# Kernel optimization log

Measured on AMD Instinct MI355X. Metric: run time of the kernel, lower is better.

## Reference

```python
import jax, jax.numpy as jnp
import numpy as np

B, N, D, O, K, E = 16, 10000, 128, 64, 3, 160000


def setup_inputs() -> dict:
    key = jax.random.key(0)
    k1, k2, k3, k4, k5 = jax.random.split(key, 5)
    x = jax.random.normal(k1, (B, N, D), dtype=jnp.float32)
    W = jax.random.normal(k2, (K, D, O), dtype=jnp.float32) * (1.0 / np.sqrt(D))
    sup_vals = jax.random.uniform(k3, (K, E), dtype=jnp.float32)
    sup_row = jax.random.randint(k4, (K, E), 0, N, dtype=jnp.int32)
    sup_col = jax.random.randint(k5, (K, E), 0, N, dtype=jnp.int32)
    return {"x": x, "W": W, "sup_vals": sup_vals, "sup_row": sup_row, "sup_col": sup_col}


def reference(x, W, sup_vals, sup_row, sup_col):
    # x: [B, N, D]; W: [K, D, O]; supports as COO edge lists per support.
    # dropout=0.0 (keep_prob=1) -> identity; act=None -> identity; agg='concat'.
    num_nodes = x.shape[1]
    num_supports = W.shape[0]
    outs = []
    for i in range(num_supports):
        # dense feature transform, laid out node-major for the SpMM: [N, B, O]
        pre = jnp.einsum('bnd,do->nbo', x, W[i])
        # SpMM: out[r] += A[r,c] * pre[c]  via gather + segment_sum
        gathered = pre[sup_col[i]] * sup_vals[i][:, None, None]  # [E, B, O]
        agg = jax.ops.segment_sum(gathered, sup_row[i], num_segments=num_nodes)  # [N, B, O]
        outs.append(jnp.transpose(agg, (1, 0, 2)))  # [B, N, O]
    return jnp.concatenate(outs, axis=-1)  # [B, N, O*K]
```

## Files before the change

kernel.cpp:

```cpp
#include <hip/hip_runtime.h>
#include <hip/hip_bf16.h>

constexpr int B = 16, N = 10000, D = 128, O = 64, K = 3, E = 160000;
constexpr int BO = B * O;
constexpr int KO = K * O;
constexpr int BSPL = 4;
constexpr int BPB  = B / BSPL;
constexpr int G = 8;
constexpr int ROWS = 8;
constexpr int NCH = N / ROWS;
constexpr int SPMM_BLOCKS = 2048;
constexpr int SLOTS_PER_XCD = (SPMM_BLOCKS / 8) * 4;

using short8  = __attribute__((ext_vector_type(8))) short;
using floatx4 = __attribute__((ext_vector_type(4))) float;
using f32x2   = __attribute__((ext_vector_type(2))) float;
struct U4 { unsigned a, b, c, d; };

__device__ __forceinline__ float bf2f(unsigned short u) {
  return __uint_as_float(((unsigned int)u) << 16);
}
__device__ __forceinline__ unsigned short f2bf(float f) {
  return (unsigned short)((__float_as_uint(f) + 0x8000u) >> 16);
}
__device__ __forceinline__ unsigned cvtpk(float lo, float hi) {
  unsigned r;
  asm("v_cvt_pk_bf16_f32 %0, %1, %2" : "=v"(r) : "v"(lo), "v"(hi));
  return r;
}

__global__ void wpack_kernel(const float* __restrict__ w, unsigned short* __restrict__ wp) {
  const int i = blockIdx.x * 64 + threadIdx.x;
  if (i >= K * 16 * 64) return;
  const int lane = i & 63;
  const int dd = (i >> 6) & 3;
  const int t4 = (i >> 8) & 3;
  const int k  = i >> 10;
  const int o  = t4 * 16 + (lane & 15);
  const int d0 = dd * 32 + (lane >> 4) * 8;
  unsigned short* dst = wp + (size_t)i * 8;
#pragma unroll
  for (int j = 0; j < 8; ++j)
    dst[j] = f2bf(w[((size_t)k * D + d0 + j) * O + o]);
}

__global__ __launch_bounds__(192) void gemm_mfma_kernel(
    const float* __restrict__ x, const unsigned short* __restrict__ wpk,
    unsigned short* __restrict__ pre, int kBase)
{
  const int t = threadIdx.x;
  const int kloc = t >> 6;
  const int k = kBase + kloc;
  const int lane = t & 63;
  const int col  = lane & 15;
  const int quad = lane >> 4;

  short8 wfr[4][4];
#pragma unroll
  for (int t4 = 0; t4 < 4; ++t4)
#pragma unroll
    for (int dd = 0; dd < 4; ++dd)
      wfr[t4][dd] = *(const short8*)(wpk + (size_t)(((k * 4 + t4) * 4 + dd) * 64 + lane) * 8);

  const int n0 = (blockIdx.x / BSPL) * 16;
  const int b0 = (blockIdx.x % BSPL) * BPB;
  const int n  = n0 + col;

  for (int bb = 0; bb < BPB; ++bb) {
    const int b = b0 + bb;
    const float* xp = x + ((size_t)b * N + n) * D + quad * 8;
    short8 xfr[4];
#pragma unroll
    for (int dd = 0; dd < 4; ++dd) {
      const float4 lo = *(const float4*)(xp + dd * 32);
      const float4 hi = *(const float4*)(xp + dd * 32 + 4);
      U4 u;
      u.a = cvtpk(lo.x, lo.y); u.b = cvtpk(lo.z, lo.w);
      u.c = cvtpk(hi.x, hi.y); u.d = cvtpk(hi.z, hi.w);
      xfr[dd] = __builtin_bit_cast(short8, u);
    }

    floatx4 acc[4] = {};
#pragma unroll
    for (int dd = 0; dd < 4; ++dd)
#pragma unroll
      for (int t4 = 0; t4 < 4; ++t4)
        acc[t4] = __builtin_amdgcn_mfma_f32_16x16x32_bf16(wfr[t4][dd], xfr[dd], acc[t4], 0, 0, 0);

    unsigned short* pp = pre + (((size_t)kloc * N + n) << 10) + b * 64 + quad * 4;
#pragma unroll
    for (int t4 = 0; t4 < 4; ++t4) {
      uint2 pk2;
      pk2.x = cvtpk(acc[t4][0], acc[t4][1]);
      pk2.y = cvtpk(acc[t4][2], acc[t4][3]);
      *(uint2*)(pp + t4 * 16) = pk2;
    }
  }
}

__global__ void hist_kernel(const int* __restrict__ row, int* __restrict__ cnt) {
  const int i = blockIdx.x * 256 + threadIdx.x;
  if (i >= K * E) return;
  const int k = i / E;
  atomicAdd(&cnt[k * N + row[i]], 1);
}

__global__ __launch_bounds__(1024) void scan_kernel(int* __restrict__ cnt,
                                                    int* __restrict__ offs) {
  const int k = blockIdx.x;
  const int t = threadIdx.x;
  const int lane = t & 63, wid = t >> 6;
  __shared__ int wt[16];
  __shared__ int sbase;
  if (t == 0) { sbase = 0; offs[k * (N + 1)] = 0; }
  __syncthreads();

  for (int c0 = 0; c0 < N; c0 += 1024) {
    const int i = c0 + t;
    const int v = (i < N) ? cnt[k * N + i] : 0;
    int incl = v;
#pragma unroll
    for (int st = 1; st < 64; st <<= 1) {
      const int u = __shfl_up(incl, st, 64);
      if (lane >= st) incl += u;
    }
    if (lane == 63) wt[wid] = incl;
    __syncthreads();
    if (wid == 0) {
      int wv = (lane < 16) ? wt[lane] : 0;
#pragma unroll
      for (int st = 1; st < 16; st <<= 1) {
        const int u = __shfl_up(wv, st, 64);
        if (lane >= st) wv += u;
      }
      if (lane < 16) wt[lane] = wv;
    }
    __syncthreads();
    const int base = sbase + ((wid > 0) ? wt[wid - 1] : 0);
    if (i < N) {
      offs[k * (N + 1) + i + 1] = base + incl;
      cnt[k * N + i] = base + incl - v;
    }
    __syncthreads();
    if (t == 0) sbase += wt[15];
    __syncthreads();
  }
}

__global__ void scatter_kernel(const int* __restrict__ row, const int* __restrict__ col,
                               const float* __restrict__ vals,
                               int* __restrict__ cursor, int* __restrict__ scol,
                               float* __restrict__ sval) {
  const int i = blockIdx.x * 256 + threadIdx.x;
  if (i >= K * E) return;
  const int k = i / E;
  const int pos = atomicAdd(&cursor[k * N + row[i]], 1);
  scol[k * E + pos] = col[i];
  sval[k * E + pos] = vals[i];
}

__global__ __launch_bounds__(256, 8) void spmm_kernel(
    const unsigned short* __restrict__ pre, const int* __restrict__ offs,
    const int* __restrict__ scol, const float* __restrict__ sval,
    float* __restrict__ out, int kBase, int kCount)
{
  const int g    = blockIdx.x & 7;
  const int slot = (blockIdx.x >> 3) * 4 + (threadIdx.x >> 6);
  const int lane = threadIdx.x & 63;

  const int bo = g * 128 + 2 * lane;
  const int b = bo >> 6;
  const int o = bo & 63;
  const int total = kCount * NCH;

  for (int c = slot; c < total; c += SLOTS_PER_XCD) {
    const int kloc = c / NCH;
    const int nc   = c - kloc * NCH;
    const int k = kBase + kloc;

    const unsigned short* pk = pre + (((size_t)kloc * N) << 10) + bo;
    const int* cj = scol + (size_t)k * E;
    const float* vj = sval + (size_t)k * E;
    const int* op = offs + k * (N + 1) + nc * ROWS;

    int ofs[ROWS + 1];
#pragma unroll
    for (int r = 0; r <= ROWS; ++r) ofs[r] = __builtin_amdgcn_readfirstlane(op[r]);

#pragma unroll
    for (int r = 0; r < ROWS; ++r) {
      const int j0 = ofs[r];
      const int j1 = ofs[r + 1];
      float a0 = 0.f, a1 = 0.f;
      int j = j0;
      for (; j + 7 < j1; j += 8) {
        unsigned u[8]; float v[8];
#pragma unroll
        for (int i = 0; i < 8; ++i) {
          const int c2 = __builtin_amdgcn_readfirstlane(cj[j + i]);
          u[i] = *(const unsigned*)(pk + ((size_t)c2 << 10));
          v[i] = vj[j + i];
        }
#pragma unroll
        for (int i = 0; i < 8; ++i) {
          a0 += v[i] * bf2f((unsigned short)(u[i] & 0xFFFFu));
          a1 += v[i] * bf2f((unsigned short)(u[i] >> 16));
        }
      }
      for (; j < j1; ++j) {
        const int c2 = __builtin_amdgcn_readfirstlane(cj[j]);
        const float v = vj[j];
        const unsigned u = *(const unsigned*)(pk + ((size_t)c2 << 10));
        a0 += v * bf2f((unsigned short)(u & 0xFFFFu));
        a1 += v * bf2f((unsigned short)(u >> 16));
      }
      const int n = nc * ROWS + r;
      f32x2 st; st.x = a0; st.y = a1;
      __builtin_nontemporal_store(st,
          (f32x2*)(out + ((size_t)b * N + n) * KO + (size_t)k * O + o));
    }
  }
}

extern "C" void kernel_launch(void* const* d_in, const int* in_sizes, int n_in,
                              void* d_out, int out_size, void* d_ws, size_t ws_size,
                              hipStream_t stream) {
  const float* x    = (const float*)d_in[0];
  const float* w    = (const float*)d_in[1];
  const float* vals = (const float*)d_in[2];
  const int* row    = (const int*)d_in[3];
  const int* col    = (const int*)d_in[4];
  float* out        = (float*)d_out;

  char* p = (char*)d_ws;
  int* offs = (int*)p;            p += ((size_t)K * (N + 1) * 4 + 15) & ~(size_t)15;
  int* cnt  = (int*)p;            p += (size_t)K * N * 4;
  int* scol = (int*)p;            p += (size_t)K * E * 4;
  float* sval = (float*)p;        p += (size_t)K * E * 4;
  unsigned short* wpk = (unsigned short*)p; p += (size_t)K * 16 * 64 * 8 * 2;
  unsigned short* pre = (unsigned short*)p;
  const size_t fixed = (size_t)(p - (char*)d_ws);
  const size_t preFull = (size_t)K * N * BO * 2;
  const bool full = ws_size >= fixed + preFull;

  hipMemsetAsync(cnt, 0, (size_t)K * N * 4, stream);

  wpack_kernel<<<48, 64, 0, stream>>>(w, wpk);
  const int eb = (K * E + 255) / 256;
  hist_kernel<<<eb, 256, 0, stream>>>(row, cnt);
  scan_kernel<<<K, 1024, 0, stream>>>(cnt, offs);
  scatter_kernel<<<eb, 256, 0, stream>>>(row, col, vals, cnt, scol, sval);

  if (full) {
    gemm_mfma_kernel<<<(N / 16) * BSPL, 64 * K, 0, stream>>>(x, wpk, pre, 0);
    spmm_kernel<<<SPMM_BLOCKS, 256, 0, stream>>>(pre, offs, scol, sval, out, 0, K);
  } else {
    for (int k = 0; k < K; ++k) {
      gemm_mfma_kernel<<<(N / 16) * BSPL, 64, 0, stream>>>(x, wpk, pre, k);
      spmm_kernel<<<SPMM_BLOCKS, 256, 0, stream>>>(pre, offs, scol, sval, out, k, 1);
    }
  }
  (void)in_sizes; (void)n_in; (void)out_size;
}
```

Baseline: 431.0 us.

## Replace static SpMM work partition with XCC-aware atomic work queues

The SpMM kernel now reads the hardware XCC id and pulls row chunks from per-column-group atomic counters in batches, instead of a fixed strided assignment keyed on block index. Each wave starts on its own XCD's column group and then steals from the other groups, so load imbalance from uneven row lengths can even out while L2 locality per group is kept. The value loads also become nontemporal. This adds per-batch atomics and an extra memset, and the row-offset loads are no longer fully unrolled.

```diff
diff --git a/kernel.cpp b/kernel.cpp
--- a/kernel.cpp
+++ b/kernel.cpp
@@ -6,11 +6,10 @@
 constexpr int KO = K * O;
 constexpr int BSPL = 4;
 constexpr int BPB  = B / BSPL;
-constexpr int G = 8;
 constexpr int ROWS = 8;
 constexpr int NCH = N / ROWS;
 constexpr int SPMM_BLOCKS = 2048;
-constexpr int SLOTS_PER_XCD = (SPMM_BLOCKS / 8) * 4;
+constexpr int QBATCH = 4;
 
 using short8  = __attribute__((ext_vector_type(8))) short;
 using floatx4 = __attribute__((ext_vector_type(4))) float;
@@ -162,62 +161,71 @@
 __global__ __launch_bounds__(256, 8) void spmm_kernel(
     const unsigned short* __restrict__ pre, const int* __restrict__ offs,
     const int* __restrict__ scol, const float* __restrict__ sval,
-    float* __restrict__ out, int kBase, int kCount)
+    float* __restrict__ out, int* __restrict__ qcnt, int kBase, int kCount)
 {
-  const int g    = blockIdx.x & 7;
-  const int slot = (blockIdx.x >> 3) * 4 + (threadIdx.x >> 6);
+  int gx;
+  asm volatile("s_getreg_b32 %0, hwreg(HW_REG_XCC_ID)" : "=s"(gx));
   const int lane = threadIdx.x & 63;
-
-  const int bo = g * 128 + 2 * lane;
-  const int b = bo >> 6;
-  const int o = bo & 63;
   const int total = kCount * NCH;
 
-  for (int c = slot; c < total; c += SLOTS_PER_XCD) {
-    const int kloc = c / NCH;
-    const int nc   = c - kloc * NCH;
-    const int k = kBase + kloc;
-
-    const unsigned short* pk = pre + (((size_t)kloc * N) << 10) + bo;
-    const int* cj = scol + (size_t)k * E;
-    const float* vj = sval + (size_t)k * E;
-    const int* op = offs + k * (N + 1) + nc * ROWS;
-
-    int ofs[ROWS + 1];
-#pragma unroll
-    for (int r = 0; r <= ROWS; ++r) ofs[r] = __builtin_amdgcn_readfirstlane(op[r]);
-
-#pragma unroll
-    for (int r = 0; r < ROWS; ++r) {
-      const int j0 = ofs[r];
-      const int j1 = ofs[r + 1];
-      float a0 = 0.f, a1 = 0.f;
-      int j = j0;
-      for (; j + 7 < j1; j += 8) {
-        unsigned u[8]; float v[8];
-#pragma unroll
-        for (int i = 0; i < 8; ++i) {
-          const int c2 = __builtin_amdgcn_readfirstlane(cj[j + i]);
-          u[i] = *(const unsigned*)(pk + ((size_t)c2 << 10));
-          v[i] = vj[j + i];
-        }
-#pragma unroll
-        for (int i = 0; i < 8; ++i) {
-          a0 += v[i] * bf2f((unsigned short)(u[i] & 0xFFFFu));
-          a1 += v[i] * bf2f((unsigned short)(u[i] >> 16));
+  for (int gg = 0; gg < 8; ++gg) {
+    const int g = (gx + gg) & 7;
+    int* q = qcnt + (kBase * 8 + g);
+    if (gg && *(volatile const int*)q >= total) continue;
+
+    const int bo = g * 128 + 2 * lane;
+    const int b = bo >> 6;
+    const int o = bo & 63;
+
+    for (;;) {
+      int c0 = 0;
+      if (lane == 0) c0 = atomicAdd(q, QBATCH);
+      int c = __shfl(c0, 0, 64);
+      if (c >= total) break;
+      const int cend = (c + QBATCH < total) ? c + QBATCH : total;
+
+      for (; c < cend; ++c) {
+        const int kloc = c / NCH;
+        const int nc   = c - kloc * NCH;
+        const int k = kBase + kloc;
+
+        const unsigned short* pk = pre + (((size_t)kloc * N) << 10) + bo;
+        const int* cj = scol + (size_t)k * E;
+        const float* vj = sval + (size_t)k * E;
+        const int* op = offs + k * (N + 1) + nc * ROWS;
+
+        for (int r = 0; r < ROWS; ++r) {
+          const int j0 = __builtin_amdgcn_readfirstlane(op[r]);
+          const int j1 = __builtin_amdgcn_readfirstlane(op[r + 1]);
+          float a0 = 0.f, a1 = 0.f;
+          int j = j0;
+          for (; j + 7 < j1; j += 8) {
+            unsigned u[8]; float v[8];
+#pragma unroll
+            for (int i = 0; i < 8; ++i) {
+              const int c2 = __builtin_amdgcn_readfirstlane(cj[j + i]);
+              u[i] = *(const unsigned*)(pk + ((size_t)c2 << 10));
+              v[i] = __builtin_nontemporal_load(vj + j + i);
+            }
+#pragma unroll
+            for (int i = 0; i < 8; ++i) {
+              a0 += v[i] * bf2f((unsigned short)(u[i] & 0xFFFFu));
+              a1 += v[i] * bf2f((unsigned short)(u[i] >> 16));
+            }
+          }
+          for (; j < j1; ++j) {
+            const int c2 = __builtin_amdgcn_readfirstlane(cj[j]);
+            const float v = __builtin_nontemporal_load(vj + j);
+            const unsigned u = *(const unsigned*)(pk + ((size_t)c2 << 10));
+            a0 += v * bf2f((unsigned short)(u & 0xFFFFu));
+            a1 += v * bf2f((unsigned short)(u >> 16));
+          }
+          const int n = nc * ROWS + r;
+          f32x2 st; st.x = a0; st.y = a1;
+          __builtin_nontemporal_store(st,
+              (f32x2*)(out + ((size_t)b * N + n) * KO + (size_t)k * O + o));
         }
       }
-      for (; j < j1; ++j) {
-        const int c2 = __builtin_amdgcn_readfirstlane(cj[j]);
-        const float v = vj[j];
-        const unsigned u = *(const unsigned*)(pk + ((size_t)c2 << 10));
-        a0 += v * bf2f((unsigned short)(u & 0xFFFFu));
-        a1 += v * bf2f((unsigned short)(u >> 16));
-      }
-      const int n = nc * ROWS + r;
-      f32x2 st; st.x = a0; st.y = a1;
-      __builtin_nontemporal_store(st,
-          (f32x2*)(out + ((size_t)b * N + n) * KO + (size_t)k * O + o));
     }
   }
 }
@@ -233,6 +241,7 @@
   float* out        = (float*)d_out;
 
   char* p = (char*)d_ws;
+  int* qcnt = (int*)p;            p += 128;
   int* offs = (int*)p;            p += ((size_t)K * (N + 1) * 4 + 15) & ~(size_t)15;
   int* cnt  = (int*)p;            p += (size_t)K * N * 4;
   int* scol = (int*)p;            p += (size_t)K * E * 4;
@@ -243,6 +252,7 @@
   const size_t preFull = (size_t)K * N * BO * 2;
   const bool full = ws_size >= fixed + preFull;
 
+  hipMemsetAsync(qcnt, 0, 128, stream);
   hipMemsetAsync(cnt, 0, (size_t)K * N * 4, stream);
 
   wpack_kernel<<<48, 64, 0, stream>>>(w, wpk);
@@ -253,11 +263,11 @@
 
   if (full) {
     gemm_mfma_kernel<<<(N / 16) * BSPL, 64 * K, 0, stream>>>(x, wpk, pre, 0);
-    spmm_kernel<<<SPMM_BLOCKS, 256, 0, stream>>>(pre, offs, scol, sval, out, 0, K);
+    spmm_kernel<<<SPMM_BLOCKS, 256, 0, stream>>>(pre, offs, scol, sval, out, qcnt, 0, K);
   } else {
     for (int k = 0; k < K; ++k) {
       gemm_mfma_kernel<<<(N / 16) * BSPL, 64, 0, stream>>>(x, wpk, pre, k);
-      spmm_kernel<<<SPMM_BLOCKS, 256, 0, stream>>>(pre, offs, scol, sval, out, k, 1);
+      spmm_kernel<<<SPMM_BLOCKS, 256, 0, stream>>>(pre, offs, scol, sval, out, qcnt, k, 1);
     }
   }
   (void)in_sizes; (void)n_in; (void)out_size;
```

Result: slower. 1.176 ms (+172.9%).

## Launch one single-wave block per SpMM work item and unroll gather by 16

Applied to the files above, without the earlier changes.

Replaces the persistent grid-stride SpMM (2048 blocks of 4 waves looping over slots) with a launch of one 64-thread block per (support, row-chunk, column-group) item, 30000 blocks in all, so the hardware scheduler does load balancing. The edge loop gains a 16-wide unrolled stage ahead of the 8-wide one, putting more independent gathers in flight per wave. The aim is to cut tail imbalance from uneven row degrees and to hide gather latency. The cost is extra block launch and scheduling overhead, more registers per thread, and the loss of the explicit launch-bounds occupancy hint.

```diff
diff --git a/kernel.cpp b/kernel.cpp
--- a/kernel.cpp
+++ b/kernel.cpp
@@ -9,8 +9,6 @@
 constexpr int G = 8;
 constexpr int ROWS = 8;
 constexpr int NCH = N / ROWS;
-constexpr int SPMM_BLOCKS = 2048;
-constexpr int SLOTS_PER_XCD = (SPMM_BLOCKS / 8) * 4;
 
 using short8  = __attribute__((ext_vector_type(8))) short;
 using floatx4 = __attribute__((ext_vector_type(4))) float;
@@ -159,66 +157,75 @@
   sval[k * E + pos] = vals[i];
 }
 
-__global__ __launch_bounds__(256, 8) void spmm_kernel(
+__global__ __launch_bounds__(64) void spmm_kernel(
     const unsigned short* __restrict__ pre, const int* __restrict__ offs,
     const int* __restrict__ scol, const float* __restrict__ sval,
-    float* __restrict__ out, int kBase, int kCount)
+    float* __restrict__ out, int kBase)
 {
-  const int g    = blockIdx.x & 7;
-  const int slot = (blockIdx.x >> 3) * 4 + (threadIdx.x >> 6);
-  const int lane = threadIdx.x & 63;
+  const int bid = blockIdx.x;
+  const int g   = bid & 7;
+  const int t2  = bid >> 3;
+  const int nc  = t2 % NCH;
+  const int kloc = t2 / NCH;
+  const int k = kBase + kloc;
+  const int lane = threadIdx.x;
 
   const int bo = g * 128 + 2 * lane;
   const int b = bo >> 6;
   const int o = bo & 63;
-  const int total = kCount * NCH;
-
-  for (int c = slot; c < total; c += SLOTS_PER_XCD) {
-    const int kloc = c / NCH;
-    const int nc   = c - kloc * NCH;
-    const int k = kBase + kloc;
-
-    const unsigned short* pk = pre + (((size_t)kloc * N) << 10) + bo;
-    const int* cj = scol + (size_t)k * E;
-    const float* vj = sval + (size_t)k * E;
-    const int* op = offs + k * (N + 1) + nc * ROWS;
-
-    int ofs[ROWS + 1];
-#pragma unroll
-    for (int r = 0; r <= ROWS; ++r) ofs[r] = __builtin_amdgcn_readfirstlane(op[r]);
-
-#pragma unroll
-    for (int r = 0; r < ROWS; ++r) {
-      const int j0 = ofs[r];
-      const int j1 = ofs[r + 1];
-      float a0 = 0.f, a1 = 0.f;
-      int j = j0;
-      for (; j + 7 < j1; j += 8) {
-        unsigned u[8]; float v[8];
-#pragma unroll
-        for (int i = 0; i < 8; ++i) {
-          const int c2 = __builtin_amdgcn_readfirstlane(cj[j + i]);
-          u[i] = *(const unsigned*)(pk + ((size_t)c2 << 10));
-          v[i] = vj[j + i];
-        }
-#pragma unroll
-        for (int i = 0; i < 8; ++i) {
-          a0 += v[i] * bf2f((unsigned short)(u[i] & 0xFFFFu));
-          a1 += v[i] * bf2f((unsigned short)(u[i] >> 16));
-        }
-      }
-      for (; j < j1; ++j) {
-        const int c2 = __builtin_amdgcn_readfirstlane(cj[j]);
-        const float v = vj[j];
-        const unsigned u = *(const unsigned*)(pk + ((size_t)c2 << 10));
-        a0 += v * bf2f((unsigned short)(u & 0xFFFFu));
-        a1 += v * bf2f((unsigned short)(u >> 16));
-      }
-      const int n = nc * ROWS + r;
-      f32x2 st; st.x = a0; st.y = a1;
-      __builtin_nontemporal_store(st,
-          (f32x2*)(out + ((size_t)b * N + n) * KO + (size_t)k * O + o));
-    }
+  const unsigned short* pk = pre + (((size_t)kloc * N) << 10) + bo;
+  const int* cj = scol + (size_t)k * E;
+  const float* vj = sval + (size_t)k * E;
+  const int* op = offs + k * (N + 1) + nc * ROWS;
+
+  int ofs[ROWS + 1];
+#pragma unroll
+  for (int r = 0; r <= ROWS; ++r) ofs[r] = __builtin_amdgcn_readfirstlane(op[r]);
+
+  for (int r = 0; r < ROWS; ++r) {
+    const int j0 = ofs[r];
+    const int j1 = ofs[r + 1];
+    float a0 = 0.f, a1 = 0.f;
+    int j = j0;
+    for (; j + 15 < j1; j += 16) {
+      unsigned u[16]; float v[16];
+#pragma unroll
+      for (int i = 0; i < 16; ++i) {
+        const int c2 = __builtin_amdgcn_readfirstlane(cj[j + i]);
+        u[i] = *(const unsigned*)(pk + ((size_t)c2 << 10));
+        v[i] = vj[j + i];
+      }
+#pragma unroll
+      for (int i = 0; i < 16; ++i) {
+        a0 += v[i] * bf2f((unsigned short)(u[i] & 0xFFFFu));
+        a1 += v[i] * bf2f((unsigned short)(u[i] >> 16));
+      }
+    }
+    for (; j + 7 < j1; j += 8) {
+      unsigned u[8]; float v[8];
+#pragma unroll
+      for (int i = 0; i < 8; ++i) {
+        const int c2 = __builtin_amdgcn_readfirstlane(cj[j + i]);
+        u[i] = *(const unsigned*)(pk + ((size_t)c2 << 10));
+        v[i] = vj[j + i];
+      }
+#pragma unroll
+      for (int i = 0; i < 8; ++i) {
+        a0 += v[i] * bf2f((unsigned short)(u[i] & 0xFFFFu));
+        a1 += v[i] * bf2f((unsigned short)(u[i] >> 16));
+      }
+    }
+    for (; j < j1; ++j) {
+      const int c2 = __builtin_amdgcn_readfirstlane(cj[j]);
+      const float v = vj[j];
+      const unsigned u = *(const unsigned*)(pk + ((size_t)c2 << 10));
+      a0 += v * bf2f((unsigned short)(u & 0xFFFFu));
+      a1 += v * bf2f((unsigned short)(u >> 16));
+    }
+    const int n = nc * ROWS + r;
+    f32x2 st; st.x = a0; st.y = a1;
+    __builtin_nontemporal_store(st,
+        (f32x2*)(out + ((size_t)b * N + n) * KO + (size_t)k * O + o));
   }
 }
 
@@ -253,11 +260,11 @@
 
   if (full) {
     gemm_mfma_kernel<<<(N / 16) * BSPL, 64 * K, 0, stream>>>(x, wpk, pre, 0);
-    spmm_kernel<<<SPMM_BLOCKS, 256, 0, stream>>>(pre, offs, scol, sval, out, 0, K);
+    spmm_kernel<<<K * NCH * G, 64, 0, stream>>>(pre, offs, scol, sval, out, 0);
   } else {
     for (int k = 0; k < K; ++k) {
       gemm_mfma_kernel<<<(N / 16) * BSPL, 64, 0, stream>>>(x, wpk, pre, k);
-      spmm_kernel<<<SPMM_BLOCKS, 256, 0, stream>>>(pre, offs, scol, sval, out, k, 1);
+      spmm_kernel<<<NCH * G, 64, 0, stream>>>(pre, offs, scol, sval, out, k);
     }
   }
   (void)in_sizes; (void)n_in; (void)out_size;
```

Measured after the change: 395.0 us. 1.09x faster.
